# Kernel optimization log

Measured on AMD Instinct MI355X. Metric: run time of the kernel, lower is better.

The kernel has to match this reference:

```python
import jax, jax.numpy as jnp
import numpy as np

H, W, D = 256, 256, 256
N_BOXES = 2048


def setup_inputs() -> dict:
    key = jax.random.key(0)
    k1, k2 = jax.random.split(key)
    feat_map = jax.random.normal(k1, (H, W, D), dtype=jnp.float32)
    # normalized boxes with x1<=x2, y1<=y2, all in [0, 1)
    xy = jax.random.uniform(k2, (N_BOXES, 2, 2), dtype=jnp.float32, maxval=0.999)
    xy = jnp.sort(xy, axis=-1)  # [..., 0] = lo, [..., 1] = hi
    boxes = jnp.stack([xy[:, 0, 0], xy[:, 1, 0], xy[:, 0, 1], xy[:, 1, 1]], axis=-1)  # [n,4] = x1,y1,x2,y2
    return {"feat_map": feat_map, "boxes": boxes}


def _bounds(lo_f, hi_f, size):
    # lo = max(0, int(lo_f*size)); hi = min(size, max(lo+1, round(hi_f*size + 0.5)))
    lo = jnp.maximum(0, jnp.floor(lo_f * size).astype(jnp.int32))
    hi = jnp.round(hi_f * size + 0.5).astype(jnp.int32)  # jnp.round = half-to-even, same as Python round
    hi = jnp.minimum(size, jnp.maximum(lo + 1, hi))
    return lo, hi


def reference(feat_map, boxes):
    h, w, d = feat_map.shape
    x1, y1, x2, y2 = boxes[:, 0], boxes[:, 1], boxes[:, 2], boxes[:, 3]
    col_lo, col_hi = _bounds(x1, x2, w)  # [n]
    row_lo, row_hi = _bounds(y1, y2, h)  # [n]

    rows = jnp.arange(h)
    cols = jnp.arange(w)
    rmask = ((rows[None, :] >= row_lo[:, None]) & (rows[None, :] < row_hi[:, None])).astype(feat_map.dtype)  # [n,H]
    cmask = ((cols[None, :] >= col_lo[:, None]) & (cols[None, :] < col_hi[:, None])).astype(feat_map.dtype)  # [n,W]

    region_sum = jnp.einsum('nh,nw,hwd->nd', rmask, cmask, feat_map)  # [n,D]
    count = ((row_hi - row_lo) * (col_hi - col_lo)).astype(feat_map.dtype)  # [n], always >= 1
    return region_sum / count[:, None]
```

## Files before the change

kernel.cpp:

```cpp
#include <hip/hip_runtime.h>

constexpr int Hh = 256;
constexpr int Ww = 256;
constexpr int Dd = 256;
constexpr int NB = 2048;

__global__ void __launch_bounds__(256) sat_row_prefix(const float* __restrict__ feat,
                                                      float* __restrict__ sat) {
    int t = blockIdx.x * blockDim.x + threadIdx.x;
    int h = t >> 8;
    int d = t & 255;
    const float* src = feat + ((size_t)h * Ww) * Dd + d;
    float*       dst = sat  + ((size_t)h * Ww) * Dd + d;
    float acc = 0.0f;
#pragma unroll 8
    for (int w = 0; w < Ww; ++w) {
        acc += src[(size_t)w * Dd];
        dst[(size_t)w * Dd] = acc;
    }
}

__global__ void __launch_bounds__(256) sat_col_prefix(float* __restrict__ sat) {
    int t = blockIdx.x * blockDim.x + threadIdx.x;
    int w = t >> 8;
    int d = t & 255;
    float* p = sat + ((size_t)w) * Dd + d;
    float acc = 0.0f;
#pragma unroll 8
    for (int h = 0; h < Hh; ++h) {
        float* q = p + (size_t)h * Ww * Dd;
        acc += *q;
        *q = acc;
    }
}

__global__ void __launch_bounds__(256) roi_pool_sat(const float* __restrict__ sat,
                                                    const float* __restrict__ boxes,
                                                    float* __restrict__ out) {
    int t = blockIdx.x * blockDim.x + threadIdx.x;
    int n = t >> 8;
    int d = t & 255;

    float x1 = boxes[n * 4 + 0];
    float y1 = boxes[n * 4 + 1];
    float x2 = boxes[n * 4 + 2];
    float y2 = boxes[n * 4 + 3];

    int cl = max(0, (int)floorf(x1 * 256.0f));
    int ch = (int)rintf(x2 * 256.0f + 0.5f);
    ch = min(Ww, max(cl + 1, ch));

    int rl = max(0, (int)floorf(y1 * 256.0f));
    int rh = (int)rintf(y2 * 256.0f + 0.5f);
    rh = min(Hh, max(rl + 1, rh));

    const float* Sbr = sat + (((size_t)(rh - 1) * Ww) + (ch - 1)) * Dd + d;
    float s = *Sbr;
    if (cl > 0) s -= sat[(((size_t)(rh - 1) * Ww) + (cl - 1)) * Dd + d];
    if (rl > 0) {
        s -= sat[(((size_t)(rl - 1) * Ww) + (ch - 1)) * Dd + d];
        if (cl > 0) s += sat[(((size_t)(rl - 1) * Ww) + (cl - 1)) * Dd + d];
    }

    float count = (float)((rh - rl) * (ch - cl));
    out[(size_t)n * Dd + d] = s / count;
}

__global__ void __launch_bounds__(256) roi_pool_naive(const float* __restrict__ feat,
                                                      const float* __restrict__ boxes,
                                                      float* __restrict__ out) {
    int n = blockIdx.x;
    int d = threadIdx.x;

    float x1 = boxes[n * 4 + 0];
    float y1 = boxes[n * 4 + 1];
    float x2 = boxes[n * 4 + 2];
    float y2 = boxes[n * 4 + 3];

    int cl = max(0, (int)floorf(x1 * 256.0f));
    int ch = (int)rintf(x2 * 256.0f + 0.5f);
    ch = min(Ww, max(cl + 1, ch));
    int rl = max(0, (int)floorf(y1 * 256.0f));
    int rh = (int)rintf(y2 * 256.0f + 0.5f);
    rh = min(Hh, max(rl + 1, rh));

    float s = 0.0f;
    for (int r = rl; r < rh; ++r) {
        const float* row = feat + ((size_t)r * Ww) * Dd + d;
        for (int c = cl; c < ch; ++c) s += row[(size_t)c * Dd];
    }
    float count = (float)((rh - rl) * (ch - cl));
    out[(size_t)n * Dd + d] = s / count;
}

extern "C" void kernel_launch(void* const* d_in, const int* in_sizes, int n_in,
                              void* d_out, int out_size, void* d_ws, size_t ws_size,
                              hipStream_t stream) {
    const float* feat  = (const float*)d_in[0];
    const float* boxes = (const float*)d_in[1];
    float* out = (float*)d_out;

    const size_t sat_bytes = (size_t)Hh * Ww * Dd * sizeof(float);

    if (ws_size >= sat_bytes) {
        float* sat = (float*)d_ws;
        sat_row_prefix<<<(Hh * Dd) / 256, 256, 0, stream>>>(feat, sat);
        sat_col_prefix<<<(Ww * Dd) / 256, 256, 0, stream>>>(sat);
        roi_pool_sat<<<(NB * Dd) / 256, 256, 0, stream>>>(sat, boxes, out);
    } else {
        roi_pool_naive<<<NB, 256, 0, stream>>>(feat, boxes, out);
    }
}
```

Baseline: 149.4 us.

## Parallelize SAT prefix scans with chunked block-level scan across spatial axis

```diff
diff --git a/kernel.cpp b/kernel.cpp
--- a/kernel.cpp
+++ b/kernel.cpp
@@ -5,33 +5,66 @@
 constexpr int Dd = 256;
 constexpr int NB = 2048;
 
-__global__ void __launch_bounds__(256) sat_row_prefix(const float* __restrict__ feat,
-                                                      float* __restrict__ sat) {
-    int t = blockIdx.x * blockDim.x + threadIdx.x;
-    int h = t >> 8;
-    int d = t & 255;
-    const float* src = feat + ((size_t)h * Ww) * Dd + d;
-    float*       dst = sat  + ((size_t)h * Ww) * Dd + d;
-    float acc = 0.0f;
-#pragma unroll 8
-    for (int w = 0; w < Ww; ++w) {
-        acc += src[(size_t)w * Dd];
-        dst[(size_t)w * Dd] = acc;
-    }
+constexpr int CH = 16;
+constexpr int NC = 16;
+constexpr int DL = 64;
+
+__global__ void __launch_bounds__(1024) sat_row_prefix(const float* __restrict__ feat,
+                                                       float* __restrict__ sat) {
+    const int tid = threadIdx.x;
+    const int dl  = tid & (DL - 1);
+    const int wc  = tid >> 6;
+    const int h   = blockIdx.x >> 2;
+    const int dq  = blockIdx.x & 3;
+    const int d   = dq * DL + dl;
+
+    const size_t base = ((size_t)h * Ww + (size_t)wc * CH) * Dd + d;
+    const float* src = feat + base;
+    float*       dst = sat + base;
+
+    float v[CH];
+#pragma unroll
+    for (int j = 0; j < CH; ++j) v[j] = src[(size_t)j * Dd];
+#pragma unroll
+    for (int j = 1; j < CH; ++j) v[j] += v[j - 1];
+
+    __shared__ float cs[NC][DL];
+    cs[wc][dl] = v[CH - 1];
+    __syncthreads();
+
+    float off = 0.0f;
+    for (int k = 0; k < wc; ++k) off += cs[k][dl];
+
+#pragma unroll
+    for (int j = 0; j < CH; ++j) dst[(size_t)j * Dd] = v[j] + off;
 }
 
-__global__ void __launch_bounds__(256) sat_col_prefix(float* __restrict__ sat) {
-    int t = blockIdx.x * blockDim.x + threadIdx.x;
-    int w = t >> 8;
-    int d = t & 255;
-    float* p = sat + ((size_t)w) * Dd + d;
-    float acc = 0.0f;
-#pragma unroll 8
-    for (int h = 0; h < Hh; ++h) {
-        float* q = p + (size_t)h * Ww * Dd;
-        acc += *q;
-        *q = acc;
-    }
+__global__ void __launch_bounds__(1024) sat_col_prefix(float* __restrict__ sat) {
+    const int tid = threadIdx.x;
+    const int dl  = tid & (DL - 1);
+    const int hc  = tid >> 6;
+    const int w   = blockIdx.x >> 2;
+    const int dq  = blockIdx.x & 3;
+    const int d   = dq * DL + dl;
+
+    float* p = sat + (size_t)w * Dd + d + (size_t)hc * CH * Ww * Dd;
+    const size_t stride = (size_t)Ww * Dd;
+
+    float v[CH];
+#pragma unroll
+    for (int j = 0; j < CH; ++j) v[j] = p[(size_t)j * stride];
+#pragma unroll
+    for (int j = 1; j < CH; ++j) v[j] += v[j - 1];
+
+    __shared__ float cs[NC][DL];
+    cs[hc][dl] = v[CH - 1];
+    __syncthreads();
+
+    float off = 0.0f;
+    for (int k = 0; k < hc; ++k) off += cs[k][dl];
+
+#pragma unroll
+    for (int j = 0; j < CH; ++j) p[(size_t)j * stride] = v[j] + off;
 }
 
 __global__ void __launch_bounds__(256) roi_pool_sat(const float* __restrict__ sat,
@@ -54,8 +87,7 @@
     int rh = (int)rintf(y2 * 256.0f + 0.5f);
     rh = min(Hh, max(rl + 1, rh));
 
-    const float* Sbr = sat + (((size_t)(rh - 1) * Ww) + (ch - 1)) * Dd + d;
-    float s = *Sbr;
+    float s = sat[(((size_t)(rh - 1) * Ww) + (ch - 1)) * Dd + d];
     if (cl > 0) s -= sat[(((size_t)(rh - 1) * Ww) + (cl - 1)) * Dd + d];
     if (rl > 0) {
         s -= sat[(((size_t)(rl - 1) * Ww) + (ch - 1)) * Dd + d];
@@ -104,8 +136,8 @@
 
     if (ws_size >= sat_bytes) {
         float* sat = (float*)d_ws;
-        sat_row_prefix<<<(Hh * Dd) / 256, 256, 0, stream>>>(feat, sat);
-        sat_col_prefix<<<(Ww * Dd) / 256, 256, 0, stream>>>(sat);
+        sat_row_prefix<<<Hh * (Dd / DL), 1024, 0, stream>>>(feat, sat);
+        sat_col_prefix<<<Ww * (Dd / DL), 1024, 0, stream>>>(sat);
         roi_pool_sat<<<(NB * Dd) / 256, 256, 0, stream>>>(sat, boxes, out);
     } else {
         roi_pool_naive<<<NB, 256, 0, stream>>>(feat, boxes, out);
```

New measurement: 125.3 us. 1.19x faster.

## Fuse column scan with ROI pooling via LDS column prefix and atomic scatter

Applied to the files above, without the earlier changes.

```diff
diff --git a/kernel.cpp b/kernel.cpp
--- a/kernel.cpp
+++ b/kernel.cpp
@@ -5,65 +5,101 @@
 constexpr int Dd = 256;
 constexpr int NB = 2048;
 
-__global__ void __launch_bounds__(256) sat_row_prefix(const float* __restrict__ feat,
-                                                      float* __restrict__ sat) {
-    int t = blockIdx.x * blockDim.x + threadIdx.x;
-    int h = t >> 8;
-    int d = t & 255;
-    const float* src = feat + ((size_t)h * Ww) * Dd + d;
-    float*       dst = sat  + ((size_t)h * Ww) * Dd + d;
-    float acc = 0.0f;
-#pragma unroll 8
-    for (int w = 0; w < Ww; ++w) {
-        acc += src[(size_t)w * Dd];
-        dst[(size_t)w * Dd] = acc;
+typedef float f4 __attribute__((ext_vector_type(4)));
+
+__global__ void __launch_bounds__(1024) k1_rowscan(const f4* __restrict__ feat,
+                                                   f4* __restrict__ pt) {
+    const int tid  = threadIdx.x;
+    const int dl   = tid & 63;
+    const int ck   = tid >> 6;
+    const int h    = blockIdx.x;
+    const int half = dl >> 5;
+    const int f    = dl & 31;
+
+    __shared__ f4 cs[16][64];
+
+    const size_t rbase = ((size_t)h * Ww + ck * 16) * 64 + dl;
+    f4 v[16];
+#pragma unroll
+    for (int j = 0; j < 16; ++j)
+        v[j] = __builtin_nontemporal_load(feat + rbase + (size_t)j * 64);
+#pragma unroll
+    for (int j = 1; j < 16; ++j) v[j] += v[j - 1];
+
+    cs[ck][dl] = v[15];
+    __syncthreads();
+    f4 off = {0.f, 0.f, 0.f, 0.f};
+    for (int k = 0; k < ck; ++k) off += cs[k][dl];
+
+#pragma unroll
+    for (int j = 0; j < 16; ++j) {
+        int w = ck * 16 + j;
+        pt[(((size_t)w * 2 + half) * Hh + h) * 32 + f] = v[j] + off;
     }
 }
 
-__global__ void __launch_bounds__(256) sat_col_prefix(float* __restrict__ sat) {
-    int t = blockIdx.x * blockDim.x + threadIdx.x;
-    int w = t >> 8;
-    int d = t & 255;
-    float* p = sat + ((size_t)w) * Dd + d;
-    float acc = 0.0f;
-#pragma unroll 8
-    for (int h = 0; h < Hh; ++h) {
-        float* q = p + (size_t)h * Ww * Dd;
-        acc += *q;
-        *q = acc;
+__global__ void __launch_bounds__(1024) k2_colscan_pool(const f4* __restrict__ pt,
+                                                        const float* __restrict__ boxes,
+                                                        float* __restrict__ out) {
+    extern __shared__ f4 lds[];
+    f4* cs   = lds;
+    f4* Cbuf = lds + 32 * 32;
+
+    const int tid  = threadIdx.x;
+    const int dl   = tid & 31;
+    const int hc   = tid >> 5;
+    const int w    = blockIdx.x >> 1;
+    const int half = blockIdx.x & 1;
+
+    const size_t base = (((size_t)w * 2 + half) * Hh + hc * 8) * 32 + dl;
+    f4 v[8];
+#pragma unroll
+    for (int j = 0; j < 8; ++j) v[j] = pt[base + (size_t)j * 32];
+#pragma unroll
+    for (int j = 1; j < 8; ++j) v[j] += v[j - 1];
+
+    cs[hc * 32 + dl] = v[7];
+    __syncthreads();
+    f4 off = {0.f, 0.f, 0.f, 0.f};
+    for (int k = 0; k < hc; ++k) off += cs[k * 32 + dl];
+
+#pragma unroll
+    for (int j = 0; j < 8; ++j) Cbuf[(hc * 8 + j) * 32 + dl] = v[j] + off;
+    __syncthreads();
+
+    for (int n = tid; n < NB; n += 1024) {
+        float x1 = boxes[n * 4 + 0];
+        float y1 = boxes[n * 4 + 1];
+        float x2 = boxes[n * 4 + 2];
+        float y2 = boxes[n * 4 + 3];
+
+        int cl = max(0, (int)floorf(x1 * 256.0f));
+        int ch = (int)rintf(x2 * 256.0f + 0.5f);
+        ch = min(Ww, max(cl + 1, ch));
+        int rl = max(0, (int)floorf(y1 * 256.0f));
+        int rh = (int)rintf(y2 * 256.0f + 0.5f);
+        rh = min(Hh, max(rl + 1, rh));
+
+        float sgn;
+        if (ch - 1 == w)      sgn =  1.0f;
+        else if (cl - 1 == w) sgn = -1.0f;
+        else continue;
+
+        float scale = sgn / (float)((rh - rl) * (ch - cl));
+        float* o = out + (size_t)n * Dd + half * 128;
+        for (int fi = 0; fi < 32; ++fi) {
+            f4 c = Cbuf[(rh - 1) * 32 + fi];
+            if (rl > 0) {
+                f4 clo = Cbuf[(rl - 1) * 32 + fi];
+                c -= clo;
+            }
+            c *= scale;
+            atomicAdd(o + fi * 4 + 0, c.x);
+            atomicAdd(o + fi * 4 + 1, c.y);
+            atomicAdd(o + fi * 4 + 2, c.z);
+            atomicAdd(o + fi * 4 + 3, c.w);
+        }
     }
-}
-
-__global__ void __launch_bounds__(256) roi_pool_sat(const float* __restrict__ sat,
-                                                    const float* __restrict__ boxes,
-                                                    float* __restrict__ out) {
-    int t = blockIdx.x * blockDim.x + threadIdx.x;
-    int n = t >> 8;
-    int d = t & 255;
-
-    float x1 = boxes[n * 4 + 0];
-    float y1 = boxes[n * 4 + 1];
-    float x2 = boxes[n * 4 + 2];
-    float y2 = boxes[n * 4 + 3];
-
-    int cl = max(0, (int)floorf(x1 * 256.0f));
-    int ch = (int)rintf(x2 * 256.0f + 0.5f);
-    ch = min(Ww, max(cl + 1, ch));
-
-    int rl = max(0, (int)floorf(y1 * 256.0f));
-    int rh = (int)rintf(y2 * 256.0f + 0.5f);
-    rh = min(Hh, max(rl + 1, rh));
-
-    const float* Sbr = sat + (((size_t)(rh - 1) * Ww) + (ch - 1)) * Dd + d;
-    float s = *Sbr;
-    if (cl > 0) s -= sat[(((size_t)(rh - 1) * Ww) + (cl - 1)) * Dd + d];
-    if (rl > 0) {
-        s -= sat[(((size_t)(rl - 1) * Ww) + (ch - 1)) * Dd + d];
-        if (cl > 0) s += sat[(((size_t)(rl - 1) * Ww) + (cl - 1)) * Dd + d];
-    }
-
-    float count = (float)((rh - rl) * (ch - cl));
-    out[(size_t)n * Dd + d] = s / count;
 }
 
 __global__ void __launch_bounds__(256) roi_pool_naive(const float* __restrict__ feat,
@@ -98,16 +134,19 @@
                               hipStream_t stream) {
     const float* feat  = (const float*)d_in[0];
     const float* boxes = (const float*)d_in[1];
-    float* out = (float*)d_out;
 
-    const size_t sat_bytes = (size_t)Hh * Ww * Dd * sizeof(float);
+    const size_t pt_bytes  = (size_t)Hh * Ww * Dd * sizeof(float);
+    const size_t lds_bytes = (32 * 32 + 256 * 32) * sizeof(f4);
 
-    if (ws_size >= sat_bytes) {
-        float* sat = (float*)d_ws;
-        sat_row_prefix<<<(Hh * Dd) / 256, 256, 0, stream>>>(feat, sat);
-        sat_col_prefix<<<(Ww * Dd) / 256, 256, 0, stream>>>(sat);
-        roi_pool_sat<<<(NB * Dd) / 256, 256, 0, stream>>>(sat, boxes, out);
+    if (ws_size >= pt_bytes) {
+        f4* pt = (f4*)d_ws;
+        hipMemsetAsync(d_out, 0, (size_t)NB * Dd * sizeof(float), stream);
+        k1_rowscan<<<Hh, 1024, 0, stream>>>((const f4*)feat, pt);
+        hipFuncSetAttribute((const void*)k2_colscan_pool,
+                            hipFuncAttributeMaxDynamicSharedMemorySize,
+                            (int)lds_bytes);
+        k2_colscan_pool<<<Ww * 2, 1024, lds_bytes, stream>>>(pt, boxes, (float*)d_out);
     } else {
-        roi_pool_naive<<<NB, 256, 0, stream>>>(feat, boxes, out);
+        roi_pool_naive<<<NB, 256, 0, stream>>>(feat, boxes, (float*)d_out);
     }
 }
```

Result: slower. 189.7 us (+27.0%).

## Replace 2D summed-area table with row prefix sums and per-box row loop

Applied to the files above, without the earlier changes.

```diff
diff --git a/kernel.cpp b/kernel.cpp
--- a/kernel.cpp
+++ b/kernel.cpp
@@ -5,41 +5,42 @@
 constexpr int Dd = 256;
 constexpr int NB = 2048;
 
-__global__ void __launch_bounds__(256) sat_row_prefix(const float* __restrict__ feat,
-                                                      float* __restrict__ sat) {
-    int t = blockIdx.x * blockDim.x + threadIdx.x;
-    int h = t >> 8;
-    int d = t & 255;
-    const float* src = feat + ((size_t)h * Ww) * Dd + d;
-    float*       dst = sat  + ((size_t)h * Ww) * Dd + d;
-    float acc = 0.0f;
-#pragma unroll 8
-    for (int w = 0; w < Ww; ++w) {
-        acc += src[(size_t)w * Dd];
-        dst[(size_t)w * Dd] = acc;
-    }
+typedef float f4 __attribute__((ext_vector_type(4)));
+
+__global__ void __launch_bounds__(256) k1_rowscan(const f4* __restrict__ feat,
+                                                  f4* __restrict__ P) {
+    const int tid = threadIdx.x;
+    const int dl  = tid & 15;
+    const int ck  = tid >> 4;
+    const int h   = blockIdx.x >> 2;
+    const int q   = blockIdx.x & 3;
+
+    __shared__ f4 cs[16][16];
+
+    const size_t base = ((size_t)h * Ww + ck * 16) * 64 + q * 16 + dl;
+    f4 v[16];
+#pragma unroll
+    for (int j = 0; j < 16; ++j)
+        v[j] = __builtin_nontemporal_load(feat + base + (size_t)j * 64);
+#pragma unroll
+    for (int j = 1; j < 16; ++j) v[j] += v[j - 1];
+
+    cs[ck][dl] = v[15];
+    __syncthreads();
+    f4 off = {0.f, 0.f, 0.f, 0.f};
+    for (int k = 0; k < ck; ++k) off += cs[k][dl];
+
+#pragma unroll
+    for (int j = 0; j < 16; ++j) P[base + (size_t)j * 64] = v[j] + off;
 }
 
-__global__ void __launch_bounds__(256) sat_col_prefix(float* __restrict__ sat) {
-    int t = blockIdx.x * blockDim.x + threadIdx.x;
-    int w = t >> 8;
-    int d = t & 255;
-    float* p = sat + ((size_t)w) * Dd + d;
-    float acc = 0.0f;
-#pragma unroll 8
-    for (int h = 0; h < Hh; ++h) {
-        float* q = p + (size_t)h * Ww * Dd;
-        acc += *q;
-        *q = acc;
-    }
-}
-
-__global__ void __launch_bounds__(256) roi_pool_sat(const float* __restrict__ sat,
-                                                    const float* __restrict__ boxes,
-                                                    float* __restrict__ out) {
-    int t = blockIdx.x * blockDim.x + threadIdx.x;
-    int n = t >> 8;
-    int d = t & 255;
+__global__ void __launch_bounds__(256) k2_boxsum(const f4* __restrict__ P,
+                                                 const float* __restrict__ boxes,
+                                                 f4* __restrict__ out) {
+    const int n    = blockIdx.x;
+    const int tid  = threadIdx.x;
+    const int dl   = tid & 63;
+    const int rsub = tid >> 6;
 
     float x1 = boxes[n * 4 + 0];
     float y1 = boxes[n * 4 + 1];
@@ -49,21 +50,37 @@
     int cl = max(0, (int)floorf(x1 * 256.0f));
     int ch = (int)rintf(x2 * 256.0f + 0.5f);
     ch = min(Ww, max(cl + 1, ch));
-
     int rl = max(0, (int)floorf(y1 * 256.0f));
     int rh = (int)rintf(y2 * 256.0f + 0.5f);
     rh = min(Hh, max(rl + 1, rh));
 
-    const float* Sbr = sat + (((size_t)(rh - 1) * Ww) + (ch - 1)) * Dd + d;
-    float s = *Sbr;
-    if (cl > 0) s -= sat[(((size_t)(rh - 1) * Ww) + (cl - 1)) * Dd + d];
-    if (rl > 0) {
-        s -= sat[(((size_t)(rl - 1) * Ww) + (ch - 1)) * Dd + d];
-        if (cl > 0) s += sat[(((size_t)(rl - 1) * Ww) + (cl - 1)) * Dd + d];
+    const int colH = ch - 1;
+    const int colL = cl - 1;
+
+    f4 acc = {0.f, 0.f, 0.f, 0.f};
+    if (colL >= 0) {
+#pragma unroll 2
+        for (int h = rl + rsub; h < rh; h += 4) {
+            f4 a = P[((size_t)h * Ww + colH) * 64 + dl];
+            f4 b = P[((size_t)h * Ww + colL) * 64 + dl];
+            acc += a - b;
+        }
+    } else {
+#pragma unroll 2
+        for (int h = rl + rsub; h < rh; h += 4) {
+            acc += P[((size_t)h * Ww + colH) * 64 + dl];
+        }
     }
 
-    float count = (float)((rh - rl) * (ch - cl));
-    out[(size_t)n * Dd + d] = s / count;
+    __shared__ f4 red[4][64];
+    red[rsub][dl] = acc;
+    __syncthreads();
+
+    if (rsub == 0) {
+        f4 s = red[0][dl] + red[1][dl] + red[2][dl] + red[3][dl];
+        float count = (float)((rh - rl) * (ch - cl));
+        out[(size_t)n * 64 + dl] = s / count;
+    }
 }
 
 __global__ void __launch_bounds__(256) roi_pool_naive(const float* __restrict__ feat,
@@ -98,16 +115,14 @@
                               hipStream_t stream) {
     const float* feat  = (const float*)d_in[0];
     const float* boxes = (const float*)d_in[1];
-    float* out = (float*)d_out;
 
-    const size_t sat_bytes = (size_t)Hh * Ww * Dd * sizeof(float);
+    const size_t p_bytes = (size_t)Hh * Ww * Dd * sizeof(float);
 
-    if (ws_size >= sat_bytes) {
-        float* sat = (float*)d_ws;
-        sat_row_prefix<<<(Hh * Dd) / 256, 256, 0, stream>>>(feat, sat);
-        sat_col_prefix<<<(Ww * Dd) / 256, 256, 0, stream>>>(sat);
-        roi_pool_sat<<<(NB * Dd) / 256, 256, 0, stream>>>(sat, boxes, out);
+    if (ws_size >= p_bytes) {
+        f4* P = (f4*)d_ws;
+        k1_rowscan<<<Hh * 4, 256, 0, stream>>>((const f4*)feat, P);
+        k2_boxsum<<<NB, 256, 0, stream>>>(P, boxes, (f4*)d_out);
     } else {
-        roi_pool_naive<<<NB, 256, 0, stream>>>(feat, boxes, out);
+        roi_pool_naive<<<NB, 256, 0, stream>>>(feat, boxes, (float*)d_out);
     }
 }
```

After: 157.2 us. 1.05x slower.
